# Kernel optimization log

Hardware: AMD Instinct MI355X
Metric: run time of the kernel (lower is better)

The kernel has to match this reference:

```python
import jax, jax.numpy as jnp
import numpy as np

B, N, M, D = 128, 256, 8, 768  # batch, input patches, memory tokens, embed dim


def setup_inputs() -> dict:
    key = jax.random.key(0)
    ks = jax.random.split(key, 6)
    w_scale = D ** -0.5
    return {
        "x": jax.random.normal(ks[0], (B, N, D), dtype=jnp.float32),
        "memory": jax.random.normal(ks[1], (M, D), dtype=jnp.float32) * 0.02,
        "Wq": jax.random.normal(ks[2], (D, D), dtype=jnp.float32) * w_scale,
        "bq": jnp.zeros((D,), dtype=jnp.float32),
        "Wk": jax.random.normal(ks[3], (D, D), dtype=jnp.float32) * w_scale,
        "bk": jnp.zeros((D,), dtype=jnp.float32),
        "Wv": jax.random.normal(ks[4], (D, D), dtype=jnp.float32) * w_scale,
        "bv": jnp.zeros((D,), dtype=jnp.float32),
        "Wo": jax.random.normal(ks[5], (D, D), dtype=jnp.float32) * w_scale,
        "bo": jnp.zeros((D,), dtype=jnp.float32),
    }


def reference(x, memory, Wq, bq, Wk, bk, Wv, bv, Wo, bo):
    b, n, d = x.shape
    m = memory.shape[0]
    t = n + m
    scaling = d ** -0.5  # mha.scaling = 1/sqrt(input_dim)
    # concat input patches with expanded memory tokens: [B, T, D]
    cat = jnp.concatenate([x, jnp.broadcast_to(memory[None], (b, m, d))], axis=1)
    q = cat @ Wq + bq
    k = cat @ Wk + bk
    v = cat @ Wv + bv
    # full attention matrix [B, T, T], softmax over keys
    att = jax.nn.softmax(jnp.einsum("bqd,bkd->bqk", q, k) * scaling, axis=-1)
    # post-softmax multiplicative mask: zero all rows for memory-token queries
    row_mask = (jnp.arange(t) < n).astype(att.dtype)[None, :, None]  # [1, T, 1]
    att = att * row_mask
    head_out = jnp.einsum("bqk,bkd->bqd", att, v)
    attended = head_out @ Wo + bo
    # return only the input-patch part (split(...)[0])
    return attended[:, :n, :]
```

## Files before the change

### kernel.cpp

```cpp
#include <hip/hip_runtime.h>
#include <hip/hip_bf16.h>

typedef __attribute__((ext_vector_type(4))) float f32x4;
typedef __attribute__((ext_vector_type(8))) short short8;
typedef __attribute__((ext_vector_type(4))) unsigned short us4;
typedef unsigned short u16;

#define DEVI __device__ __forceinline__

#define BB 128
#define NN 256
#define MMEM 8
#define DD 768
#define TT 264
#define TP 320
#define SP 384
#define AROWS2 33024

DEVI u16 f2bf(float f) {
  __hip_bfloat16 b = __float2bfloat16(f);
  u16 u; __builtin_memcpy(&u, &b, 2); return u;
}

DEVI void gload_lds16(const void* g, void* l) {
  __builtin_amdgcn_global_load_lds((const __attribute__((address_space(1))) void*)g,
                                   (__attribute__((address_space(3))) void*)l, 16, 0, 0);
}


__global__ __launch_bounds__(256)
void conv_x(const float* __restrict__ x, const float* __restrict__ mem, u16* __restrict__ Ab) {
  const long total4 = (long)AROWS2 * DD / 4;
  for (long i = (long)blockIdx.x * blockDim.x + threadIdx.x; i < total4;
       i += (long)gridDim.x * blockDim.x) {
    long e = i * 4;
    int row = (int)(e / DD);
    int cb  = (int)(e % DD);
    f32x4 v = {0.f, 0.f, 0.f, 0.f};
    if (row < BB * NN)             v = *(const f32x4*)(x   + (size_t)row * DD + cb);
    else if (row < BB * NN + MMEM) v = *(const f32x4*)(mem + (size_t)(row - BB * NN) * DD + cb);
    us4 o = {f2bf(v[0]), f2bf(v[1]), f2bf(v[2]), f2bf(v[3])};
    *(us4*)(Ab + e) = o;
  }
}

__global__ __launch_bounds__(256)
void conv_w(const float* __restrict__ Wq, const float* __restrict__ Wk,
            const float* __restrict__ Wv, const float* __restrict__ Wo,
            u16* __restrict__ Wqt, u16* __restrict__ Wkt,
            u16* __restrict__ Wvt, u16* __restrict__ Wot) {
  const int total = 4 * DD * DD;
  for (int i = blockIdx.x * blockDim.x + threadIdx.x; i < total;
       i += gridDim.x * blockDim.x) {
    int mat = i / (DD * DD), rem = i % (DD * DD);
    int j = rem / DD, d = rem % DD;
    const float* W = (mat == 0) ? Wq : (mat == 1) ? Wk : (mat == 2) ? Wv : Wo;
    u16* Wt = (mat == 0) ? Wqt : (mat == 1) ? Wkt : (mat == 2) ? Wvt : Wot;
    Wt[(size_t)j * DD + d] = f2bf(W[(size_t)d * DD + j]);
  }
}


#define BAR()   __builtin_amdgcn_s_barrier()
#define SCB()   __builtin_amdgcn_sched_barrier(0)
#define LGKM0() asm volatile("s_waitcnt lgkmcnt(0)" ::: "memory")
#define VM4()   asm volatile("s_waitcnt vmcnt(4)" ::: "memory")

#define STG(gb, isB, ss, rg, kt) do {                                          \
    const u16* _s = (gb) + (size_t)((rg) * 16 + srow) * DD + (kt) * 64 + scol; \
    char* _d = smem + (ss) * 65536 + (isB) * 32768 + (rg) * 2048;              \
    gload_lds16(_s, _d);                                                       \
    gload_lds16(_s + 32, _d + 1024);                                           \
  } while (0)

#define STG_A0(ss, kt) STG(Ab, 0, ss, ((w & 3) | ((w & 4) << 1)), kt)
#define STG_B0(ss, kt) STG(Bb, 1, ss, ((w & 1) | ((w & 6) << 1)), kt)
#define STG_A1(ss, kt) STG(Ab, 0, ss, (((w & 3) | ((w & 4) << 1)) + 4), kt)
#define STG_B1(ss, kt) STG(Bb, 1, ss, (((w & 1) | ((w & 6) << 1)) + 2), kt)

#define RD_A(dst, s, QM)                                                          \
  _Pragma("unroll") for (int mi = 0; mi < 4; ++mi)                                \
  _Pragma("unroll") for (int ks = 0; ks < 2; ++ks)                                \
    dst[mi][ks] = *(const short8*)(smem + (s) * 65536 +                           \
                    ((wm * 8 + (QM) * 4 + mi) * 2 + ks) * 1024 + fbase);

#define RD_B(dst, s, QN)                                                          \
  _Pragma("unroll") for (int ni = 0; ni < 2; ++ni)                                \
  _Pragma("unroll") for (int ks = 0; ks < 2; ++ks)                                \
    dst[ni][ks] = *(const short8*)(smem + (s) * 65536 + 32768 +                   \
                    ((wn * 4 + (QN) * 2 + ni) * 2 + ks) * 1024 + fbase);

#define MM(FA, FB, QM, QN)                                                        \
  _Pragma("unroll") for (int mi = 0; mi < 4; ++mi)                                \
  _Pragma("unroll") for (int ni = 0; ni < 2; ++ni)                                \
  _Pragma("unroll") for (int ks = 0; ks < 2; ++ks)                                \
    acc[(QM)*4+mi][(QN)*2+ni] = __builtin_amdgcn_mfma_f32_16x16x32_bf16(          \
        FA[mi][ks], FB[ni][ks], acc[(QM)*4+mi][(QN)*2+ni], 0, 0, 0);

template<int MODE>
__global__ __launch_bounds__(512)
void gemm256(const u16* __restrict__ A, const u16* __restrict__ Bq,
             const u16* __restrict__ Bk, const u16* __restrict__ Bv,
             const float* __restrict__ b0, const float* __restrict__ b1,
             const float* __restrict__ b2,
             u16* __restrict__ Oq, u16* __restrict__ Ok, u16* __restrict__ Ov,
             float* __restrict__ FO, int NT)
{
  extern __shared__ char smem[];
  const int tid = threadIdx.x;
  const int l = tid & 63;
  const int w = tid >> 6;
  const int wm = w >> 2, wn = w & 3;

  const int nwg = gridDim.x * gridDim.y;
  const int lin = blockIdx.y * gridDim.x + blockIdx.x;
  const int qq = nwg >> 3, rr = nwg & 7;
  const int xcd = lin & 7, idx = lin >> 3;
  const int wg = (xcd < rr ? xcd * (qq + 1) : rr * (qq + 1) + (xcd - rr) * qq) + idx;
  const int tn = wg % gridDim.x, tm = wg / gridDim.x;

  const u16* Ab = A + (size_t)tm * 256 * DD;
  const u16* Bb;
  int matsel = 0;
  if constexpr (MODE == 0) {
    matsel = tn / 3;
    const u16* Wp = (matsel == 0) ? Bq : (matsel == 1) ? Bk : Bv;
    Bb = Wp + (size_t)(tn % 3) * 256 * DD;
  } else {
    Bb = Bq + (size_t)tn * 256 * DD;
  }

  const int jj = (l < 32) ? l : (l ^ 2);
  const int srow = jj >> 2;
  const int scol = (jj & 3) * 8;
  const int fbase = (((l & 15) * 64) + ((l >> 4) * 16)) ^ (((l >> 3) & 1) << 5);

  f32x4 acc[8][4];
  #pragma unroll
  for (int i = 0; i < 8; ++i)
    #pragma unroll
    for (int jx = 0; jx < 4; ++jx) acc[i][jx] = (f32x4){0.f, 0.f, 0.f, 0.f};

  short8 fa0[4][2], fa1[4][2], fb0[2][2], fb1[2][2];

  STG_A0(0, 0); STG_B0(0, 0); STG_A1(0, 0); STG_B1(0, 0);
  VM4(); BAR();

  for (int g = 0; g < NT; ++g) {
    const int s = g & 1, ss = s ^ 1;
    const int st = (g + 1 < NT) ? (g + 1) : 0;

    RD_A(fa0, s, 0); RD_B(fb0, s, 0);
    STG_A0(ss, st);
    BAR(); LGKM0(); SCB();
    __builtin_amdgcn_s_setprio(1); MM(fa0, fb0, 0, 0); __builtin_amdgcn_s_setprio(0);
    VM4(); BAR();

    RD_A(fa1, s, 1);
    STG_B0(ss, st);
    BAR(); LGKM0(); SCB();
    __builtin_amdgcn_s_setprio(1); MM(fa1, fb0, 1, 0); __builtin_amdgcn_s_setprio(0);
    VM4(); BAR();

    RD_B(fb1, s, 1);
    STG_A1(ss, st);
    BAR(); LGKM0(); SCB();
    __builtin_amdgcn_s_setprio(1); MM(fa1, fb1, 1, 1); __builtin_amdgcn_s_setprio(0);
    BAR();

    STG_B1(ss, st);
    BAR(); LGKM0(); SCB();
    __builtin_amdgcn_s_setprio(1); MM(fa0, fb1, 0, 1); __builtin_amdgcn_s_setprio(0);
    VM4(); BAR();
  }

  const int fr = l & 15, fro = (l >> 4) * 4;
  if constexpr (MODE == 0) {
    const float* bias = (matsel == 0) ? b0 : (matsel == 1) ? b1 : b2;
    u16* ob = (matsel == 0) ? Oq : (matsel == 1) ? Ok : Ov;
    const int cb = (tn % 3) * 256 + wn * 64;
    const size_t rb = (size_t)tm * 256 + wm * 128;
    #pragma unroll
    for (int MI = 0; MI < 8; ++MI)
      #pragma unroll
      for (int NI = 0; NI < 4; ++NI) {
        const int col = cb + NI * 16 + fr;
        const float bvv = bias[col];
        #pragma unroll
        for (int r = 0; r < 4; ++r)
          ob[(rb + MI * 16 + fro + r) * DD + col] = f2bf(acc[MI][NI][r] + bvv);
      }
  } else {
    const int cb = tn * 256 + wn * 64;
    const size_t rb = (size_t)tm * 256 + wm * 128;
    #pragma unroll
    for (int MI = 0; MI < 8; ++MI)
      #pragma unroll
      for (int NI = 0; NI < 4; ++NI) {
        const int col = cb + NI * 16 + fr;
        const float bvv = b0[col];
        #pragma unroll
        for (int r = 0; r < 4; ++r)
          FO[(rb + MI * 16 + fro + r) * DD + col] = acc[MI][NI][r] + bvv;
      }
  }
}


template<int MODE>
__global__ __launch_bounds__(256)
void gemm_bt(const u16* __restrict__ A, const u16* __restrict__ Bm,
             const float* __restrict__ f0,
             u16* __restrict__ U0, float* __restrict__ F0, int Kdim)
{
  const int tid = threadIdx.x;
  const int l  = tid & 63;
  const int w  = tid >> 6;
  const int wm = w >> 1, wn = w & 1;
  const int tm = blockIdx.x, tn = blockIdx.y, z = blockIdx.z;

  __shared__ u16 lsA[128 * 32];
  __shared__ u16 lsB[128 * 32];

  const u16* Abase; int lda;
  if constexpr (MODE == 1)      { Abase = A + ((size_t)z * NN + tm * 128) * DD; lda = DD; }
  else                          { Abase = A + ((size_t)z * NN + tm * 128) * TP; lda = TP; }

  const u16* Bbase; int ldb;
  if constexpr (MODE == 1) { Bbase = Bm; ldb = DD; }
  else                     { Bbase = Bm + ((size_t)z * DD + tn * 128) * TP; ldb = TP; }

  f32x4 acc[4][4];
  #pragma unroll
  for (int i = 0; i < 4; i++)
    #pragma unroll
    for (int j = 0; j < 4; j++) acc[i][j] = (f32x4){0.f, 0.f, 0.f, 0.f};

  const int srow = l >> 2;
  const int scol = (l & 3) * 8;
  const int nkt = Kdim >> 5;

  for (int kt = 0; kt < nkt; ++kt) {
    const int kpos = kt * 32 + scol;
    #pragma unroll
    for (int q = 0; q < 2; ++q) {
      const int r = q * 64 + w * 16 + srow;
      gload_lds16(Abase + (size_t)r * lda + kpos, &lsA[q * 2048 + w * 512]);
    }
    #pragma unroll
    for (int q = 0; q < 2; ++q) {
      const int r = q * 64 + w * 16 + srow;
      const u16* src;
      if constexpr (MODE == 1) {
        const int t = tn * 128 + r;
        const int rr = (t < NN) ? (z * NN + t)
                     : ((t < TT) ? (BB * NN + t - NN) : BB * NN);
        src = Bm + (size_t)rr * DD + kpos;
      } else {
        src = Bbase + (size_t)r * ldb + kpos;
      }
      gload_lds16(src, &lsB[q * 2048 + w * 512]);
    }
    __syncthreads();

    const int fr = l & 15, fk = (l >> 4) * 8;
    short8 fa[4], fb[4];
    #pragma unroll
    for (int mi = 0; mi < 4; mi++)
      fa[mi] = *(const short8*)&lsA[(wm * 64 + mi * 16 + fr) * 32 + fk];
    #pragma unroll
    for (int ni = 0; ni < 4; ni++)
      fb[ni] = *(const short8*)&lsB[(wn * 64 + ni * 16 + fr) * 32 + fk];
    #pragma unroll
    for (int mi = 0; mi < 4; mi++)
      #pragma unroll
      for (int ni = 0; ni < 4; ni++)
        acc[mi][ni] = __builtin_amdgcn_mfma_f32_16x16x32_bf16(fa[mi], fb[ni], acc[mi][ni], 0, 0, 0);
    __syncthreads();
  }

  const int fr  = l & 15;
  const int fro = (l >> 4) * 4;

  if constexpr (MODE == 1) {
    const float scl = 0.03608439182435161f;
    float* Sb = F0 + (size_t)z * NN * SP;
    const int cb = tn * 128 + wn * 64;
    const int rb = tm * 128 + wm * 64;
    #pragma unroll
    for (int mi = 0; mi < 4; mi++)
      #pragma unroll
      for (int ni = 0; ni < 4; ni++)
        #pragma unroll
        for (int r = 0; r < 4; r++)
          Sb[(size_t)(rb + mi * 16 + fro + r) * SP + cb + ni * 16 + fr] = acc[mi][ni][r] * scl;
  } else {
    const int cb = tn * 128 + wn * 64;
    const size_t rb = (size_t)z * NN + tm * 128 + wm * 64;
    #pragma unroll
    for (int mi = 0; mi < 4; mi++)
      #pragma unroll
      for (int ni = 0; ni < 4; ni++)
        #pragma unroll
        for (int r = 0; r < 4; r++)
          U0[(rb + mi * 16 + fro + r) * DD + cb + ni * 16 + fr] = f2bf(acc[mi][ni][r]);
  }
}


__global__ __launch_bounds__(256)
void softmax_k(const float* __restrict__ S, u16* __restrict__ P) {
  const int l = threadIdx.x & 63;
  const int row = blockIdx.x * 4 + (threadIdx.x >> 6);
  const float* s = S + (size_t)row * SP;
  float v0 = s[l], v1 = s[64 + l], v2 = s[128 + l], v3 = s[192 + l];
  float v4 = (l < 8) ? s[256 + l] : -__builtin_inff();
  float m = fmaxf(fmaxf(fmaxf(v0, v1), fmaxf(v2, v3)), v4);
  #pragma unroll
  for (int off = 32; off; off >>= 1) m = fmaxf(m, __shfl_xor(m, off));
  float e0 = __expf(v0 - m), e1 = __expf(v1 - m), e2 = __expf(v2 - m), e3 = __expf(v3 - m);
  float e4 = (l < 8) ? __expf(v4 - m) : 0.f;
  float sum = e0 + e1 + e2 + e3 + e4;
  #pragma unroll
  for (int off = 32; off; off >>= 1) sum += __shfl_xor(sum, off);
  const float inv = 1.f / sum;
  u16* p = P + (size_t)row * TP;
  p[l] = f2bf(e0 * inv); p[64 + l] = f2bf(e1 * inv);
  p[128 + l] = f2bf(e2 * inv); p[192 + l] = f2bf(e3 * inv);
  if (l < 8) p[256 + l] = f2bf(e4 * inv);
  else       p[256 + l] = 0;
}


__global__ __launch_bounds__(256)
void transpose_v(const u16* __restrict__ V, u16* __restrict__ Vt) {
  __shared__ u16 ls[64 * 66];
  const int b = blockIdx.z;
  const int d0 = blockIdx.x * 64;
  const int t0 = blockIdx.y * 64;
  const int tid = threadIdx.x;
  #pragma unroll
  for (int q = 0; q < 2; ++q) {
    const int idx = q * 256 + tid;
    const int tr = idx >> 3;
    const int dg = (idx & 7) * 8;
    const int t = t0 + tr;
    short8 v = (short8)(short)0;
    if (t < NN)       v = *(const short8*)(V + ((size_t)b * NN + t) * DD + d0 + dg);
    else if (t < TT)  v = *(const short8*)(V + (size_t)(BB * NN + t - NN) * DD + d0 + dg);
    #pragma unroll
    for (int e = 0; e < 8; ++e) ls[tr * 66 + dg + e] = (u16)v[e];
  }
  __syncthreads();
  #pragma unroll
  for (int q = 0; q < 2; ++q) {
    const int idx = q * 256 + tid;
    const int dr = idx >> 3;
    const int tg = (idx & 7) * 8;
    short8 v;
    #pragma unroll
    for (int e = 0; e < 8; ++e) v[e] = (short)ls[(tg + e) * 66 + dr];
    *(short8*)(Vt + ((size_t)b * DD + d0 + dr) * TP + t0 + tg) = v;
  }
}


extern "C" void kernel_launch(void* const* d_in, const int* in_sizes, int n_in,
                              void* d_out, int out_size, void* d_ws, size_t ws_size,
                              hipStream_t stream) {
  const float* x   = (const float*)d_in[0];
  const float* mem = (const float*)d_in[1];
  const float* Wq  = (const float*)d_in[2];
  const float* bq  = (const float*)d_in[3];
  const float* Wk  = (const float*)d_in[4];
  const float* bk  = (const float*)d_in[5];
  const float* Wv  = (const float*)d_in[6];
  const float* bv  = (const float*)d_in[7];
  const float* Wo  = (const float*)d_in[8];
  const float* bo  = (const float*)d_in[9];
  float* out = (float*)d_out;
  (void)ws_size; (void)in_sizes; (void)n_in; (void)out_size;

  const size_t QKV_B = (size_t)AROWS2 * DD * 2;
  char* wsb = (char*)d_ws;
  u16* Qb  = (u16*)(wsb);
  u16* Kb  = (u16*)(wsb + QKV_B);
  u16* Vb  = (u16*)(wsb + 2 * QKV_B);
  u16* Vt  = (u16*)(wsb);
  u16* O   = (u16*)(wsb + (size_t)BB * DD * TP * 2);
  u16* Wot = (u16*)(wsb + 3 * QKV_B);

  u16*   Ab  = (u16*)d_out;
  float* S   = (float*)d_out;
  u16*   P   = (u16*)((char*)d_out + QKV_B);
  u16*   Wqt = (u16*)((char*)d_out + 97124352);
  u16*   Wkt = Wqt + (size_t)DD * DD;
  u16*   Wvt = Wkt + (size_t)DD * DD;

  conv_x<<<2048, 256, 0, stream>>>(x, mem, Ab);
  conv_w<<<1024, 256, 0, stream>>>(Wq, Wk, Wv, Wo, Wqt, Wkt, Wvt, Wot);

  gemm256<0><<<dim3(9, 129), 512, 131072, stream>>>(
      Ab, Wqt, Wkt, Wvt, bq, bk, bv, Qb, Kb, Vb, nullptr, DD / 64);

  gemm_bt<1><<<dim3(2, 3, BB), 256, 0, stream>>>(Qb, Kb, nullptr, nullptr, S, DD);

  softmax_k<<<8192, 256, 0, stream>>>(S, P);

  transpose_v<<<dim3(12, 5, BB), 256, 0, stream>>>(Vb, Vt);

  gemm_bt<2><<<dim3(2, 6, BB), 256, 0, stream>>>(P, Vt, nullptr, O, nullptr, TP);

  gemm256<1><<<dim3(3, 128), 512, 131072, stream>>>(
      O, Wot, nullptr, nullptr, bo, nullptr, nullptr,
      nullptr, nullptr, nullptr, out, DD / 64);
}
```

Before: 349.1 us.

## Fuse QK^T, softmax and PV into one attention kernel per query tile

Replaces the separate score GEMM, softmax kernel and P·V GEMM with a single fused kernel. Each 512-thread block computes a 128×272 score tile in registers, applies softmax in registers, and stores bf16 probabilities in LDS. It then streams V^T chunks through double-buffered LDS for the P·V product. This removes the fp32 score matrix and bf16 P round trips through global memory, plus two launches. In exchange it uses large LDS per block, only 256 blocks, and heavy register pressure from the 17 score accumulators and 24 output accumulators.

Result: slower. 367.2 us (+5.2%).

```diff
diff --git a/kernel.cpp b/kernel.cpp
--- a/kernel.cpp
+++ b/kernel.cpp
@@ -14,7 +14,6 @@
 #define DD 768
 #define TT 264
 #define TP 320
-#define SP 384
 #define AROWS2 33024
 
 DEVI u16 f2bf(float f) {
@@ -65,6 +64,8 @@
 #define SCB()   __builtin_amdgcn_sched_barrier(0)
 #define LGKM0() asm volatile("s_waitcnt lgkmcnt(0)" ::: "memory")
 #define VM4()   asm volatile("s_waitcnt vmcnt(4)" ::: "memory")
+#define VMW0()  asm volatile("s_waitcnt vmcnt(0)" ::: "memory")
+#define VMW3()  asm volatile("s_waitcnt vmcnt(3)" ::: "memory")
 
 #define STG(gb, isB, ss, rg, kt) do {                                          \
     const u16* _s = (gb) + (size_t)((rg) * 16 + srow) * DD + (kt) * 64 + scol; \
@@ -207,131 +208,6 @@
 }
 
 
-template<int MODE>
-__global__ __launch_bounds__(256)
-void gemm_bt(const u16* __restrict__ A, const u16* __restrict__ Bm,
-             const float* __restrict__ f0,
-             u16* __restrict__ U0, float* __restrict__ F0, int Kdim)
-{
-  const int tid = threadIdx.x;
-  const int l  = tid & 63;
-  const int w  = tid >> 6;
-  const int wm = w >> 1, wn = w & 1;
-  const int tm = blockIdx.x, tn = blockIdx.y, z = blockIdx.z;
-
-  __shared__ u16 lsA[128 * 32];
-  __shared__ u16 lsB[128 * 32];
-
-  const u16* Abase; int lda;
-  if constexpr (MODE == 1)      { Abase = A + ((size_t)z * NN + tm * 128) * DD; lda = DD; }
-  else                          { Abase = A + ((size_t)z * NN + tm * 128) * TP; lda = TP; }
-
-  const u16* Bbase; int ldb;
-  if constexpr (MODE == 1) { Bbase = Bm; ldb = DD; }
-  else                     { Bbase = Bm + ((size_t)z * DD + tn * 128) * TP; ldb = TP; }
-
-  f32x4 acc[4][4];
-  #pragma unroll
-  for (int i = 0; i < 4; i++)
-    #pragma unroll
-    for (int j = 0; j < 4; j++) acc[i][j] = (f32x4){0.f, 0.f, 0.f, 0.f};
-
-  const int srow = l >> 2;
-  const int scol = (l & 3) * 8;
-  const int nkt = Kdim >> 5;
-
-  for (int kt = 0; kt < nkt; ++kt) {
-    const int kpos = kt * 32 + scol;
-    #pragma unroll
-    for (int q = 0; q < 2; ++q) {
-      const int r = q * 64 + w * 16 + srow;
-      gload_lds16(Abase + (size_t)r * lda + kpos, &lsA[q * 2048 + w * 512]);
-    }
-    #pragma unroll
-    for (int q = 0; q < 2; ++q) {
-      const int r = q * 64 + w * 16 + srow;
-      const u16* src;
-      if constexpr (MODE == 1) {
-        const int t = tn * 128 + r;
-        const int rr = (t < NN) ? (z * NN + t)
-                     : ((t < TT) ? (BB * NN + t - NN) : BB * NN);
-        src = Bm + (size_t)rr * DD + kpos;
-      } else {
-        src = Bbase + (size_t)r * ldb + kpos;
-      }
-      gload_lds16(src, &lsB[q * 2048 + w * 512]);
-    }
-    __syncthreads();
-
-    const int fr = l & 15, fk = (l >> 4) * 8;
-    short8 fa[4], fb[4];
-    #pragma unroll
-    for (int mi = 0; mi < 4; mi++)
-      fa[mi] = *(const short8*)&lsA[(wm * 64 + mi * 16 + fr) * 32 + fk];
-    #pragma unroll
-    for (int ni = 0; ni < 4; ni++)
-      fb[ni] = *(const short8*)&lsB[(wn * 64 + ni * 16 + fr) * 32 + fk];
-    #pragma unroll
-    for (int mi = 0; mi < 4; mi++)
-      #pragma unroll
-      for (int ni = 0; ni < 4; ni++)
-        acc[mi][ni] = __builtin_amdgcn_mfma_f32_16x16x32_bf16(fa[mi], fb[ni], acc[mi][ni], 0, 0, 0);
-    __syncthreads();
-  }
-
-  const int fr  = l & 15;
-  const int fro = (l >> 4) * 4;
-
-  if constexpr (MODE == 1) {
-    const float scl = 0.03608439182435161f;
-    float* Sb = F0 + (size_t)z * NN * SP;
-    const int cb = tn * 128 + wn * 64;
-    const int rb = tm * 128 + wm * 64;
-    #pragma unroll
-    for (int mi = 0; mi < 4; mi++)
-      #pragma unroll
-      for (int ni = 0; ni < 4; ni++)
-        #pragma unroll
-        for (int r = 0; r < 4; r++)
-          Sb[(size_t)(rb + mi * 16 + fro + r) * SP + cb + ni * 16 + fr] = acc[mi][ni][r] * scl;
-  } else {
-    const int cb = tn * 128 + wn * 64;
-    const size_t rb = (size_t)z * NN + tm * 128 + wm * 64;
-    #pragma unroll
-    for (int mi = 0; mi < 4; mi++)
-      #pragma unroll
-      for (int ni = 0; ni < 4; ni++)
-        #pragma unroll
-        for (int r = 0; r < 4; r++)
-          U0[(rb + mi * 16 + fro + r) * DD + cb + ni * 16 + fr] = f2bf(acc[mi][ni][r]);
-  }
-}
-
-
-__global__ __launch_bounds__(256)
-void softmax_k(const float* __restrict__ S, u16* __restrict__ P) {
-  const int l = threadIdx.x & 63;
-  const int row = blockIdx.x * 4 + (threadIdx.x >> 6);
-  const float* s = S + (size_t)row * SP;
-  float v0 = s[l], v1 = s[64 + l], v2 = s[128 + l], v3 = s[192 + l];
-  float v4 = (l < 8) ? s[256 + l] : -__builtin_inff();
-  float m = fmaxf(fmaxf(fmaxf(v0, v1), fmaxf(v2, v3)), v4);
-  #pragma unroll
-  for (int off = 32; off; off >>= 1) m = fmaxf(m, __shfl_xor(m, off));
-  float e0 = __expf(v0 - m), e1 = __expf(v1 - m), e2 = __expf(v2 - m), e3 = __expf(v3 - m);
-  float e4 = (l < 8) ? __expf(v4 - m) : 0.f;
-  float sum = e0 + e1 + e2 + e3 + e4;
-  #pragma unroll
-  for (int off = 32; off; off >>= 1) sum += __shfl_xor(sum, off);
-  const float inv = 1.f / sum;
-  u16* p = P + (size_t)row * TP;
-  p[l] = f2bf(e0 * inv); p[64 + l] = f2bf(e1 * inv);
-  p[128 + l] = f2bf(e2 * inv); p[192 + l] = f2bf(e3 * inv);
-  if (l < 8) p[256 + l] = f2bf(e4 * inv);
-  else       p[256 + l] = 0;
-}
-
-
 __global__ __launch_bounds__(256)
 void transpose_v(const u16* __restrict__ V, u16* __restrict__ Vt) {
   __shared__ u16 ls[64 * 66];
@@ -361,6 +237,171 @@
     #pragma unroll
     for (int e = 0; e < 8; ++e) v[e] = (short)ls[(tg + e) * 66 + dr];
     *(short8*)(Vt + ((size_t)b * DD + d0 + dr) * TP + t0 + tg) = v;
+  }
+}
+
+
+#define PPITCH 592
+#define POFF   51200
+#define VSLOT  24576
+
+__global__ __launch_bounds__(512)
+void fused_attn(const u16* __restrict__ Qb, const u16* __restrict__ Kb,
+                const u16* __restrict__ Vt, u16* __restrict__ O)
+{
+  extern __shared__ char smem[];
+  const int tid = threadIdx.x;
+  const int l = tid & 63;
+  const int w = tid >> 6;
+  const int qt = blockIdx.x;
+  const int b  = blockIdx.y;
+
+  const int jj = (l < 32) ? l : (l ^ 2);
+  const int srow = jj >> 2;
+  const int scol = (jj & 3) * 8;
+  const int fbase = (((l & 15) * 64) + ((l >> 4) * 16)) ^ (((l >> 3) & 1) << 5);
+  const int fr = l & 15, g4 = l >> 4;
+
+  f32x4 accS[17];
+  #pragma unroll
+  for (int i = 0; i < 17; ++i) accS[i] = (f32x4){0.f, 0.f, 0.f, 0.f};
+
+  const u16* Qrow0 = Qb + ((size_t)b * NN + qt * 128) * DD;
+
+  for (int kt = 0; kt < 12; ++kt) {
+    const int kpos = kt * 64 + scol;
+    {
+      const u16* src = Qrow0 + (size_t)(w * 16 + srow) * DD + kpos;
+      char* dst = smem + w * 2048;
+      gload_lds16(src, dst); gload_lds16(src + 32, dst + 1024);
+    }
+    #pragma unroll
+    for (int rep = 0; rep < 2; ++rep) {
+      const int rg = w + rep * 8;
+      const int kr = rg * 16 + srow;
+      const int grow = (kr < NN) ? (b * NN + kr) : (BB * NN + kr - NN);
+      const u16* src = Kb + (size_t)grow * DD + kpos;
+      char* dst = smem + 16384 + rg * 2048;
+      gload_lds16(src, dst); gload_lds16(src + 32, dst + 1024);
+    }
+    if (w == 0) {
+      const int grow = BB * NN + srow;
+      const u16* src = Kb + (size_t)grow * DD + kpos;
+      char* dst = smem + 16384 + 16 * 2048;
+      gload_lds16(src, dst); gload_lds16(src + 32, dst + 1024);
+    }
+    VMW0(); BAR();
+
+    short8 aq0 = *(const short8*)(smem + (w * 2 + 0) * 1024 + fbase);
+    short8 aq1 = *(const short8*)(smem + (w * 2 + 1) * 1024 + fbase);
+    #pragma unroll
+    for (int ni = 0; ni < 17; ++ni) {
+      short8 bk0 = *(const short8*)(smem + 16384 + (ni * 2 + 0) * 1024 + fbase);
+      short8 bk1 = *(const short8*)(smem + 16384 + (ni * 2 + 1) * 1024 + fbase);
+      accS[ni] = __builtin_amdgcn_mfma_f32_16x16x32_bf16(aq0, bk0, accS[ni], 0, 0, 0);
+      accS[ni] = __builtin_amdgcn_mfma_f32_16x16x32_bf16(aq1, bk1, accS[ni], 0, 0, 0);
+    }
+    BAR();
+  }
+
+  const float scl = 0.03608439182435161f;
+  #pragma unroll
+  for (int ni = 0; ni < 17; ++ni) {
+    #pragma unroll
+    for (int r = 0; r < 4; ++r) accS[ni][r] *= scl;
+  }
+  if (fr >= 8) {
+    #pragma unroll
+    for (int r = 0; r < 4; ++r) accS[16][r] = -1e30f;
+  }
+  #pragma unroll
+  for (int r = 0; r < 4; ++r) {
+    float mv = -1e30f;
+    #pragma unroll
+    for (int ni = 0; ni < 17; ++ni) mv = fmaxf(mv, accS[ni][r]);
+    #pragma unroll
+    for (int off = 8; off; off >>= 1) mv = fmaxf(mv, __shfl_xor(mv, off));
+    float sum = 0.f;
+    #pragma unroll
+    for (int ni = 0; ni < 17; ++ni) {
+      float e = __expf(accS[ni][r] - mv);
+      accS[ni][r] = e;
+      sum += e;
+    }
+    #pragma unroll
+    for (int off = 8; off; off >>= 1) sum += __shfl_xor(sum, off);
+    const float inv = 1.f / sum;
+    const int q = w * 16 + g4 * 4 + r;
+    char* prow = smem + POFF + q * PPITCH;
+    #pragma unroll
+    for (int ni = 0; ni < 17; ++ni)
+      *(u16*)(prow + (ni * 16 + fr) * 2) = f2bf(accS[ni][r] * inv);
+    *(u16*)(prow + (272 + fr) * 2) = 0;
+  }
+  __syncthreads();
+
+  const u16* Vtb = Vt + (size_t)b * DD * TP;
+  const int qh = w >> 2, dq = w & 3;
+  f32x4 accO[4][6];
+
+  {
+    #pragma unroll
+    for (int rep = 0; rep < 3; ++rep) {
+      const int rg = w * 3 + rep;
+      const u16* src = Vtb + (size_t)(rg * 16 + srow) * TP + scol;
+      gload_lds16(src, smem + rg * 1024);
+    }
+  }
+
+  int cur = 0;
+  for (int p = 0; p < 2; ++p) {
+    #pragma unroll
+    for (int mi = 0; mi < 4; ++mi)
+      #pragma unroll
+      for (int nj = 0; nj < 6; ++nj) accO[mi][nj] = (f32x4){0.f, 0.f, 0.f, 0.f};
+
+    for (int tc = 0; tc < 9; ++tc) {
+      int np = p, nc = tc + 1;
+      if (nc == 9) { np = p + 1; nc = 0; }
+      if (np == 2) { np = 1; nc = 8; }
+      BAR();
+      {
+        #pragma unroll
+        for (int rep = 0; rep < 3; ++rep) {
+          const int rg = w * 3 + rep;
+          const u16* src = Vtb + (size_t)(np * 384 + rg * 16 + srow) * TP + nc * 32 + scol;
+          gload_lds16(src, smem + (cur ^ 1) * VSLOT + rg * 1024);
+        }
+      }
+      VMW3();
+      BAR();
+
+      short8 pa[4], vb[6];
+      #pragma unroll
+      for (int mi = 0; mi < 4; ++mi)
+        pa[mi] = *(const short8*)(smem + POFF +
+                   (qh * 64 + mi * 16 + fr) * PPITCH + tc * 64 + g4 * 16);
+      #pragma unroll
+      for (int nj = 0; nj < 6; ++nj)
+        vb[nj] = *(const short8*)(smem + cur * VSLOT + (dq * 6 + nj) * 1024 + fbase);
+      __builtin_amdgcn_s_setprio(1);
+      #pragma unroll
+      for (int mi = 0; mi < 4; ++mi)
+        #pragma unroll
+        for (int nj = 0; nj < 6; ++nj)
+          accO[mi][nj] = __builtin_amdgcn_mfma_f32_16x16x32_bf16(pa[mi], vb[nj], accO[mi][nj], 0, 0, 0);
+      __builtin_amdgcn_s_setprio(0);
+      cur ^= 1;
+    }
+
+    u16* Ob = O + ((size_t)b * NN + qt * 128 + qh * 64) * DD + p * 384 + dq * 96;
+    #pragma unroll
+    for (int mi = 0; mi < 4; ++mi)
+      #pragma unroll
+      for (int nj = 0; nj < 6; ++nj)
+        #pragma unroll
+        for (int r = 0; r < 4; ++r)
+          Ob[(size_t)(mi * 16 + g4 * 4 + r) * DD + nj * 16 + fr] = f2bf(accO[mi][nj][r]);
   }
 }
 
@@ -386,13 +427,11 @@
   u16* Qb  = (u16*)(wsb);
   u16* Kb  = (u16*)(wsb + QKV_B);
   u16* Vb  = (u16*)(wsb + 2 * QKV_B);
-  u16* Vt  = (u16*)(wsb);
-  u16* O   = (u16*)(wsb + (size_t)BB * DD * TP * 2);
+  u16* O   = (u16*)(wsb + 2 * QKV_B);
   u16* Wot = (u16*)(wsb + 3 * QKV_B);
 
   u16*   Ab  = (u16*)d_out;
-  float* S   = (float*)d_out;
-  u16*   P   = (u16*)((char*)d_out + QKV_B);
+  u16*   Vt  = (u16*)d_out;
   u16*   Wqt = (u16*)((char*)d_out + 97124352);
   u16*   Wkt = Wqt + (size_t)DD * DD;
   u16*   Wvt = Wkt + (size_t)DD * DD;
@@ -403,13 +442,9 @@
   gemm256<0><<<dim3(9, 129), 512, 131072, stream>>>(
       Ab, Wqt, Wkt, Wvt, bq, bk, bv, Qb, Kb, Vb, nullptr, DD / 64);
 
-  gemm_bt<1><<<dim3(2, 3, BB), 256, 0, stream>>>(Qb, Kb, nullptr, nullptr, S, DD);
-
-  softmax_k<<<8192, 256, 0, stream>>>(S, P);
-
   transpose_v<<<dim3(12, 5, BB), 256, 0, stream>>>(Vb, Vt);
 
-  gemm_bt<2><<<dim3(2, 6, BB), 256, 0, stream>>>(P, Vt, nullptr, O, nullptr, TP);
+  fused_attn<<<dim3(2, BB), 512, 126976, stream>>>(Qb, Kb, Vt, O);
 
   gemm256<1><<<dim3(3, 128), 512, 131072, stream>>>(
       O, Wot, nullptr, nullptr, bo, nullptr, nullptr,
```
